# Performance work log

Measured on AMD Instinct MI355X. Metric: run time of the kernel, lower is better.

Reference implementation:

```python
import jax, jax.numpy as jnp
import numpy as np

NUM_HEADS = 16
D_MODEL = 1024
HEAD_DIM = D_MODEL // NUM_HEADS
EPS = 1e-6


def setup_inputs() -> dict:
    key = jax.random.key(0)
    ks = jax.random.split(key, 9)
    B, S, D = 4, 8192, D_MODEL
    scale = 1.0 / np.sqrt(D)  # variance_scaling(1.0, fan_in, normal) approx
    inputs_q = jax.random.normal(ks[0], (B, S, D), dtype=jnp.float32)
    Wq = jax.random.normal(ks[1], (D, D), dtype=jnp.float32) * scale
    Wk = jax.random.normal(ks[2], (D, D), dtype=jnp.float32) * scale
    Wv = jax.random.normal(ks[3], (D, D), dtype=jnp.float32) * scale
    Wo = jax.random.normal(ks[4], (D, D), dtype=jnp.float32) * scale
    bq = jnp.zeros((D,), jnp.float32)
    bk = jnp.zeros((D,), jnp.float32)
    bv = jnp.zeros((D,), jnp.float32)
    bo = jnp.zeros((D,), jnp.float32)
    return {"inputs_q": inputs_q, "Wq": Wq, "bq": bq, "Wk": Wk, "bk": bk,
            "Wv": Wv, "bv": bv, "Wo": Wo, "bo": bo}


def _feature_map(x):
    return jax.nn.elu(x) + 1.0


def reference(inputs_q, Wq, bq, Wk, bk, Wv, bv, Wo, bo):
    B, S, D = inputs_q.shape
    H, Dh = NUM_HEADS, HEAD_DIM
    # QKV projections (self-attention: k,v inputs default to q input)
    q = (inputs_q @ Wq + bq).reshape(B, S, H, Dh)
    k = (inputs_q @ Wk + bk).reshape(B, S, H, Dh)
    v = (inputs_q @ Wv + bv).reshape(B, S, H, Dh)
    q = _feature_map(q)
    k = _feature_map(k)
    # KV outer-product accumulation: [B, H, Dh, Dh]
    kv = jnp.einsum('bkhd,bkhm->bhdm', k, v)
    out = jnp.einsum('bqhd,bhdm->bqhm', q, kv)
    # normalizer: q . sum_k(k)
    normalizer = jnp.einsum('bqhd,bkhd->bqh', q, k)
    normalizer = jnp.maximum(normalizer, EPS)
    out = out / normalizer[..., None]
    out = out.reshape(B, S, D)
    return out @ Wo + bo
```

## Files before the change

kernel.cpp:

```cpp
#include <hip/hip_runtime.h>
#include <cstdint>
#include <cstddef>

#define D_MODEL 1024
#define SEQ 8192

typedef __bf16  bf16x8 __attribute__((ext_vector_type(8)));
typedef short   short8 __attribute__((ext_vector_type(8)));
typedef float   f32x4  __attribute__((ext_vector_type(4)));
typedef unsigned short ushort_t;

__device__ __forceinline__ ushort_t f2bf(float f) {
  uint32_t u = __builtin_bit_cast(uint32_t, f);
  u += 0x7FFFu + ((u >> 16) & 1u);
  return (ushort_t)(u >> 16);
}
__device__ __forceinline__ void gll16(const void* g, void* l) {
  __builtin_amdgcn_global_load_lds(
      (const __attribute__((address_space(1))) void*)g,
      (__attribute__((address_space(3))) void*)l, 16, 0, 0);
}
__device__ __forceinline__ void stage_half(const ushort_t* g, char* l0) {
  gll16(g, l0);
  gll16(g + 65536, l0 + 8192);
}

__global__ void k_convert_x(const float* __restrict__ x, ushort_t* __restrict__ xb, int n) {
  int i = (blockIdx.x * 256 + threadIdx.x) * 8;
  if (i >= n) return;
  float4 v0 = *(const float4*)(x + i);
  float4 v1 = *(const float4*)(x + i + 4);
  ushort_t o[8] = { f2bf(v0.x), f2bf(v0.y), f2bf(v0.z), f2bf(v0.w),
                    f2bf(v1.x), f2bf(v1.y), f2bf(v1.z), f2bf(v1.w) };
  *(short8*)(xb + i) = *(const short8*)o;
}

__global__ void k_transpose_w(const float* W0, const float* W1, const float* W2, const float* W3,
                              ushort_t* Tqkv, ushort_t* To) {
  const float* src; ushort_t* dst;
  switch (blockIdx.z) {
    case 0: src = W0; dst = Tqkv; break;
    case 1: src = W1; dst = Tqkv + (size_t)1024 * 1024; break;
    case 2: src = W2; dst = Tqkv + (size_t)2048 * 1024; break;
    default: src = W3; dst = To; break;
  }
  __shared__ float tile[64][65];
  int tx = threadIdx.x;
  int c = tx & 63, r0 = tx >> 6;
  int bx = blockIdx.x * 64, by = blockIdx.y * 64;
  #pragma unroll
  for (int i = 0; i < 16; i++) {
    int r = i * 4 + r0;
    tile[r][c] = src[(size_t)(by + r) * D_MODEL + bx + c];
  }
  __syncthreads();
  #pragma unroll
  for (int i = 0; i < 16; i++) {
    int r = i * 4 + r0;
    dst[(size_t)(bx + r) * D_MODEL + by + c] = f2bf(tile[c][r]);
  }
}

template<int MODE, int NY>
__global__ __launch_bounds__(512, 2) void k_gemm(const ushort_t* __restrict__ A,
                                                 const ushort_t* __restrict__ Bt,
                                                 const float* __restrict__ b0,
                                                 const float* __restrict__ b1,
                                                 const float* __restrict__ b2,
                                                 ushort_t* __restrict__ o0,
                                                 ushort_t* __restrict__ o1,
                                                 ushort_t* __restrict__ o2,
                                                 float* __restrict__ outf) {
  __shared__ __align__(16) char smem[131072];

  const int nwg = gridDim.x;
  const int bid0 = blockIdx.x;
  const int bid = (bid0 & 7) * (nwg >> 3) + (bid0 >> 3);
  const int xb = bid / NY, yb = bid % NY;
  const int m0 = xb * 256, n0 = yb * 256;

  const int tid = threadIdx.x;
  const int ln = tid & 63;
  const int w  = tid >> 6;
  const int wb = __builtin_amdgcn_readfirstlane(w);
  const int wm = wb >> 2, wn = wb & 3;

  const int srow = wb * 8 + (ln >> 3);
  const int schk = ((ln & 7) ^ ((ln >> 3) & 7)) * 8;
  const ushort_t* gA = A  + (size_t)(m0 + srow) * D_MODEL + schk;
  const ushort_t* gB = Bt + (size_t)(n0 + srow) * D_MODEL + schk;

#define STG_A(BASE, H, T) stage_half(gA + (size_t)(T) * 64 + (size_t)(H) * 131072, smem + (BASE) + (H) * 16384 + wb * 1024)
#define STG_B(BASE, H, T) stage_half(gB + (size_t)(T) * 64 + (size_t)(H) * 131072, smem + (BASE) + 32768 + (H) * 16384 + wb * 1024)

#define VMW_(N) asm volatile("s_waitcnt vmcnt(" #N ")" ::: "memory")
#define VMW(N)  VMW_(N)
#define LGW_(N) asm volatile("s_waitcnt lgkmcnt(" #N ")" ::: "memory")
#define LGW__(N) LGW_(N)
#define LGW(N)  do { LGW__(N); __builtin_amdgcn_sched_barrier(0); } while (0)
#define BARSB { __builtin_amdgcn_s_barrier(); __builtin_amdgcn_sched_barrier(0); }

  f32x4 acc[8][4];
  #pragma unroll
  for (int i = 0; i < 8; i++)
    #pragma unroll
    for (int j = 0; j < 4; j++) acc[i][j] = (f32x4){0.f, 0.f, 0.f, 0.f};
  bf16x8 a0f[4][2], a1f[4][2];
  bf16x8 b0f[2][2], b1f[2][2];

  const int ar  = ln & 15;
  const int cw0 = (((ln >> 4)    ) ^ (ln & 7)) << 4;
  const int cw1 = (((ln >> 4) + 4) ^ (ln & 7)) << 4;

#define LDAH(DST, BASE, MH) { _Pragma("unroll") for (int m_ = 0; m_ < 4; ++m_) { \
    const char* p_ = smem + (BASE) + ((wm * 128 + (MH) * 64 + m_ * 16 + ar) << 7); \
    DST[m_][0] = *(const bf16x8*)(p_ + cw0); DST[m_][1] = *(const bf16x8*)(p_ + cw1); } }
#define LDBH(DST, BASE, NH) { _Pragma("unroll") for (int j_ = 0; j_ < 2; ++j_) { \
    const char* p_ = smem + (BASE) + 32768 + ((wn * 64 + (NH) * 32 + j_ * 16 + ar) << 7); \
    DST[j_][0] = *(const bf16x8*)(p_ + cw0); DST[j_][1] = *(const bf16x8*)(p_ + cw1); } }
#define QUAD(MH, NH, AF, BF) { _Pragma("unroll") for (int m_ = 0; m_ < 4; ++m_) \
    _Pragma("unroll") for (int j_ = 0; j_ < 2; ++j_) { \
      acc[(MH)*4+m_][(NH)*2+j_] = __builtin_amdgcn_mfma_f32_16x16x32_bf16(AF[m_][0], BF[j_][0], acc[(MH)*4+m_][(NH)*2+j_], 0, 0, 0); \
      acc[(MH)*4+m_][(NH)*2+j_] = __builtin_amdgcn_mfma_f32_16x16x32_bf16(AF[m_][1], BF[j_][1], acc[(MH)*4+m_][(NH)*2+j_], 0, 0, 0); } }

#define TILE(T, BT, BN, S1, S2, R1, LP2, LP3) { \
     \
    LDAH(a1f, BT, 1); \
    if (S1) STG_B(BN, 1, (T) + 1); \
    BARSB; \
    LGW(8); \
    __builtin_amdgcn_s_setprio(1); QUAD(0, 0, a0f, b0f); __builtin_amdgcn_s_setprio(0); \
    BARSB; \
     \
    LDBH(b1f, BT, 1); \
    BARSB; \
    LGW(4); \
    __builtin_amdgcn_s_setprio(1); QUAD(1, 0, a1f, b0f); __builtin_amdgcn_s_setprio(0); \
    VMW(0); \
    BARSB; \
     \
    if (R1) LDBH(b0f, BN, 0); \
    if (S2) STG_A(BT, 0, (T) + 2); \
    BARSB; \
    LGW(LP2); \
    __builtin_amdgcn_s_setprio(1); QUAD(0, 1, a0f, b1f); __builtin_amdgcn_s_setprio(0); \
    BARSB; \
     \
    if (R1) LDAH(a0f, BN, 0); \
    if (S2) { STG_A(BT, 1, (T) + 2); STG_B(BT, 0, (T) + 2); } \
    BARSB; \
    LGW(LP3); \
    __builtin_amdgcn_s_setprio(1); QUAD(1, 1, a1f, b1f); __builtin_amdgcn_s_setprio(0); \
    BARSB; \
  }

  STG_A(0, 0, 0); STG_A(0, 1, 0); STG_B(0, 0, 0); STG_B(0, 1, 0);
  STG_A(65536, 0, 1); STG_A(65536, 1, 1); STG_B(65536, 0, 1);
  VMW(6);
  BARSB;
  LDAH(a0f, 0, 0);
  LDBH(b0f, 0, 0);

  #pragma unroll 1
  for (int kt = 0; kt < 14; kt += 2) {
    TILE(kt,     0,     65536, true, true, true, 4, 8);
    TILE(kt + 1, 65536, 0,     true, true, true, 4, 8);
  }
  TILE(14, 0,     65536, true,  false, true,  4, 8);
  TILE(15, 65536, 0,     false, false, false, 0, 0);

#undef STG_A
#undef STG_B
#undef LDAH
#undef LDBH
#undef QUAD
#undef TILE

  const int colb = ln & 15, rowb = (ln >> 4) * 4;

  if constexpr (MODE == 0) {
    const int region = yb >> 2;
    const int nl0 = (yb & 3) * 256;
    const float* bias = region == 0 ? b0 : (region == 1 ? b1 : b2);
    ushort_t* gout    = region == 0 ? o0 : (region == 1 ? o1 : o2);
    const bool act = region < 2;
    ushort_t* Cs = (ushort_t*)smem;
    #pragma unroll
    for (int j = 0; j < 4; ++j) {
      const int col = wn * 64 + j * 16 + colb;
      const float bv_ = bias[nl0 + col];
      #pragma unroll
      for (int i = 0; i < 8; ++i) {
        const int rb_ = wm * 128 + i * 16 + rowb;
        #pragma unroll
        for (int r = 0; r < 4; ++r) {
          float v = acc[i][j][r] + bv_;
          if (act) v = (v > 0.f) ? v + 1.f : __expf(v);
          const int row = rb_ + r;
          const int ch = col >> 3;
          Cs[row * 256 + ((ch ^ (row & 31)) << 3) + (col & 7)] = f2bf(v);
        }
      }
    }
    __syncthreads();
    #pragma unroll
    for (int c = 0; c < 16; ++c) {
      const int idx = c * 512 + tid;
      const int row = idx >> 5, ch = idx & 31;
      short8 t = *(const short8*)&Cs[row * 256 + ((ch ^ (row & 31)) << 3)];
      *(short8*)&gout[(size_t)(m0 + row) * D_MODEL + nl0 + ch * 8] = t;
    }
  } else {
    float* Cf = (float*)smem;
    #pragma unroll
    for (int h = 0; h < 2; ++h) {
      if (h) __syncthreads();
      if (wm == h) {
        #pragma unroll
        for (int j = 0; j < 4; ++j) {
          const int col = wn * 64 + j * 16 + colb;
          const float bv_ = b0[n0 + col];
          #pragma unroll
          for (int i = 0; i < 8; ++i) {
            const int rl = i * 16 + rowb;
            #pragma unroll
            for (int r = 0; r < 4; ++r) {
              const int row = rl + r;
              const int ch = col >> 2;
              Cf[row * 256 + ((ch ^ (row & 7)) << 2) + (col & 3)] = acc[i][j][r] + bv_;
            }
          }
        }
      }
      __syncthreads();
      #pragma unroll
      for (int c = 0; c < 16; ++c) {
        const int idx = c * 512 + tid;
        const int row = idx >> 6, ch = idx & 63;
        float4 t = *(const float4*)&Cf[row * 256 + ((ch ^ (row & 7)) << 2)];
        *(float4*)&outf[(size_t)(m0 + h * 128 + row) * D_MODEL + n0 + ch * 4] = t;
      }
    }
  }
#undef VMW_
#undef VMW
#undef LGW_
#undef LGW__
#undef LGW
#undef BARSB
}

__global__ __launch_bounds__(256) void k_kv_partial(const ushort_t* __restrict__ kmat,
                                                    const ushort_t* __restrict__ vmat,
                                                    float* __restrict__ part) {
  __shared__ __align__(16) ushort_t sbuf[4][2][2][512];
  const int tid = threadIdx.x, ln = tid & 63, w = tid >> 6;
  const int wb = __builtin_amdgcn_readfirstlane(w);
  const int bh = blockIdx.y, chunk = blockIdx.x;
  const int b = bh >> 4, h = bh & 15;
  const size_t cbase = ((size_t)b * SEQ + chunk * 1024 + w * 256) * D_MODEL + h * 64;
  const ushort_t* gk = kmat + cbase + (size_t)(ln >> 3) * D_MODEL + (ln & 7) * 8;
  const ushort_t* gv = vmat + cbase + (size_t)(ln >> 3) * D_MODEL + (ln & 7) * 8;

  float acc[8][8];
  float ksum[8];
  #pragma unroll
  for (int i = 0; i < 8; i++) { ksum[i] = 0.f;
    #pragma unroll
    for (int j = 0; j < 8; j++) acc[i][j] = 0.f; }

  const int r8 = (ln >> 3) * 8, c8 = (ln & 7) * 8;
  gll16(gk, &sbuf[wb][0][0][0]);
  gll16(gv, &sbuf[wb][0][1][0]);
  gk += 8 * D_MODEL; gv += 8 * D_MODEL;

  for (int bt = 0; bt < 32; bt++) {
    const int p = bt & 1;
    if (bt < 31) {
      gll16(gk, &sbuf[wb][p ^ 1][0][0]);
      gll16(gv, &sbuf[wb][p ^ 1][1][0]);
      gk += 8 * D_MODEL; gv += 8 * D_MODEL;
      __builtin_amdgcn_s_waitcnt(0x0F72);
    } else {
      __builtin_amdgcn_s_waitcnt(0x0F70);
    }
    #pragma unroll
    for (int s = 0; s < 8; s++) {
      short8 kk = *(const short8*)&sbuf[wb][p][0][s * 64 + r8];
      short8 vv = *(const short8*)&sbuf[wb][p][1][s * 64 + c8];
      float ka[8], va[8];
      #pragma unroll
      for (int i = 0; i < 8; i++) {
        ka[i] = __builtin_bit_cast(float, (uint32_t)(ushort_t)kk[i] << 16);
        va[i] = __builtin_bit_cast(float, (uint32_t)(ushort_t)vv[i] << 16);
      }
      #pragma unroll
      for (int i = 0; i < 8; i++) {
        ksum[i] += ka[i];
        #pragma unroll
        for (int j = 0; j < 8; j++) acc[i][j] += ka[i] * va[j];
      }
    }
  }
  float* p0 = part + ((size_t)bh * 32 + chunk * 4 + w) * 4160;
  #pragma unroll
  for (int i = 0; i < 8; i++)
    #pragma unroll
    for (int j = 0; j < 8; j++) p0[(r8 + i) * 64 + c8 + j] = acc[i][j];
  if ((ln & 7) == 0) {
    #pragma unroll
    for (int i = 0; i < 8; i++) p0[4096 + r8 + i] = ksum[i];
  }
}

__global__ void k_kv_reduce(const float* __restrict__ part, ushort_t* __restrict__ kvt) {
  const int bh = blockIdx.x, tid = threadIdx.x;
  const float* p0 = part + (size_t)bh * 32 * 4160;
  for (int idx = tid; idx < 4160; idx += 256) {
    float s = 0.f;
    #pragma unroll 4
    for (int c = 0; c < 32; c++) s += p0[(size_t)c * 4160 + idx];
    ushort_t bf = f2bf(s);
    if (idx < 4096) { int d = idx >> 6, m = idx & 63; kvt[(size_t)bh * 4160 + m * 64 + d] = bf; }
    else            { kvt[(size_t)bh * 4160 + 4096 + (idx - 4096)] = bf; }
  }
}

__global__ __launch_bounds__(256) void k_attn(const ushort_t* __restrict__ qmat,
                                              const ushort_t* __restrict__ kvt,
                                              ushort_t* __restrict__ attn) {
  __shared__ __align__(16) ushort_t kvs[65 * 80];
  __shared__ __align__(16) ushort_t qs[4][64 * 80];
  const int tid = threadIdx.x, ln = tid & 63, w = tid >> 6;
  const int bh = blockIdx.y, b = bh >> 4, h = bh & 15;

  for (int idx = tid; idx < 4160; idx += 256) {
    int m = idx >> 6, d = idx & 63;
    kvs[m * 80 + d] = kvt[(size_t)bh * 4160 + idx];
  }
  const size_t s0 = (size_t)b * SEQ + blockIdx.x * 256 + w * 64;
  #pragma unroll
  for (int c = 0; c < 8; c++) {
    int f = c * 64 + ln;
    int row = f >> 3, dg = (f & 7) * 8;
    short8 t = *(const short8*)&qmat[(s0 + row) * D_MODEL + h * 64 + dg];
    *(short8*)&qs[w][row * 80 + dg] = t;
  }
  __syncthreads();

  const int ar = ln & 15, aq = (ln >> 4) * 8;
  f32x4 acc[4][4], nacc[4];
  #pragma unroll
  for (int i = 0; i < 4; i++) { nacc[i] = (f32x4){0.f, 0.f, 0.f, 0.f};
    #pragma unroll
    for (int j = 0; j < 4; j++) acc[i][j] = (f32x4){0.f, 0.f, 0.f, 0.f}; }

  #pragma unroll
  for (int kk = 0; kk < 2; kk++) {
    const int ko = kk * 32 + aq;
    bf16x8 a[4], bb[4], bn;
    #pragma unroll
    for (int i = 0; i < 4; i++) a[i] = *(const bf16x8*)&qs[w][(i * 16 + ar) * 80 + ko];
    #pragma unroll
    for (int j = 0; j < 4; j++) bb[j] = *(const bf16x8*)&kvs[(j * 16 + ar) * 80 + ko];
    bn = *(const bf16x8*)&kvs[64 * 80 + ko];
    #pragma unroll
    for (int i = 0; i < 4; i++) {
      #pragma unroll
      for (int j = 0; j < 4; j++)
        acc[i][j] = __builtin_amdgcn_mfma_f32_16x16x32_bf16(a[i], bb[j], acc[i][j], 0, 0, 0);
      nacc[i] = __builtin_amdgcn_mfma_f32_16x16x32_bf16(a[i], bn, nacc[i], 0, 0, 0);
    }
  }

  const int colb = ln & 15, rowb = (ln >> 4) * 4;
  #pragma unroll
  for (int i = 0; i < 4; i++) {
    #pragma unroll
    for (int r = 0; r < 4; r++) {
      const int row = i * 16 + rowb + r;
      float nm = fmaxf(nacc[i][r], 1e-6f);
      float inv = 1.0f / nm;
      const size_t grow = s0 + row;
      #pragma unroll
      for (int j = 0; j < 4; j++) {
        float v = acc[i][j][r] * inv;
        attn[grow * D_MODEL + h * 64 + j * 16 + colb] = f2bf(v);
      }
    }
  }
}

extern "C" void kernel_launch(void* const* d_in, const int* in_sizes, int n_in,
                              void* d_out, int out_size, void* d_ws, size_t ws_size,
                              hipStream_t stream) {
  const float* x  = (const float*)d_in[0];
  const float* Wq = (const float*)d_in[1];
  const float* bq = (const float*)d_in[2];
  const float* Wk = (const float*)d_in[3];
  const float* bk = (const float*)d_in[4];
  const float* Wv = (const float*)d_in[5];
  const float* bv = (const float*)d_in[6];
  const float* Wo = (const float*)d_in[7];
  const float* bo = (const float*)d_in[8];
  float* out = (float*)d_out;

  const int M = in_sizes[0] / D_MODEL;
  const int B = M / SEQ;
  const int BH = B * 16;

  char* ws = (char*)d_ws;
  size_t off = 0;
  auto alloc = [&](size_t bytes) { char* p = ws + off; off += (bytes + 255) & ~(size_t)255; return p; };
  const size_t mb = (size_t)M * D_MODEL * 2;
  ushort_t* xb    = (ushort_t*)alloc(mb);
  ushort_t* qb    = (ushort_t*)alloc(mb);
  ushort_t* kb    = (ushort_t*)alloc(mb);
  ushort_t* vb    = (ushort_t*)alloc(mb);
  ushort_t* attnb = (ushort_t*)alloc(mb);
  ushort_t* wqkvt = (ushort_t*)alloc((size_t)3 * D_MODEL * D_MODEL * 2);
  ushort_t* wot   = (ushort_t*)alloc((size_t)D_MODEL * D_MODEL * 2);
  ushort_t* kvt   = (ushort_t*)alloc((size_t)BH * 4160 * 2);
  float*    part  = (float*)   alloc((size_t)BH * 32 * 4160 * 4);
  (void)ws_size; (void)n_in; (void)out_size;

  const int n = M * D_MODEL;
  k_convert_x<<<n / (256 * 8), 256, 0, stream>>>(x, xb, n);
  k_transpose_w<<<dim3(16, 16, 4), 256, 0, stream>>>(Wq, Wk, Wv, Wo, wqkvt, wot);

  k_gemm<0, 12><<<(M / 256) * 12, 512, 0, stream>>>(xb, wqkvt, bq, bk, bv, qb, kb, vb, nullptr);

  k_kv_partial<<<dim3(8, BH), 256, 0, stream>>>(kb, vb, part);
  k_kv_reduce<<<BH, 256, 0, stream>>>(part, kvt);
  k_attn<<<dim3(SEQ / 256, BH), 256, 0, stream>>>(qb, kvt, attnb);

  k_gemm<2, 4><<<(M / 256) * 4, 512, 0, stream>>>(attnb, wot, bo, nullptr, nullptr, nullptr, nullptr, nullptr, out);
}
```

Baseline: 807.9 us.

## Restructure GEMM main loop with single A fragment buffer and whole-tile prefetch

Reworks the 256x256 bf16 GEMM k-loop schedule. Each tile now loads its own A and B fragments from LDS at the start instead of prefetching the next tile's fragments during the current one. It keeps a single A fragment register set, reorders the four MFMA quadrants, and issues both halves of the next-next A and B global-to-LDS stages within the tile. This cuts register pressure (fewer fragment buffers) and simplifies wait counts. The cost is that LDS read latency is exposed at the start of each tile, with full lgkmcnt(0) waits before each quadrant.

Measured after the change: 681.6 us. 1.19x faster.

```diff
diff --git a/kernel.cpp b/kernel.cpp
--- a/kernel.cpp
+++ b/kernel.cpp
@@ -95,9 +95,8 @@
 
 #define VMW_(N) asm volatile("s_waitcnt vmcnt(" #N ")" ::: "memory")
 #define VMW(N)  VMW_(N)
-#define LGW_(N) asm volatile("s_waitcnt lgkmcnt(" #N ")" ::: "memory")
-#define LGW__(N) LGW_(N)
-#define LGW(N)  do { LGW__(N); __builtin_amdgcn_sched_barrier(0); } while (0)
+#define LGWC_(N) asm volatile("s_waitcnt lgkmcnt(" #N ")" ::: "memory")
+#define LGW0 do { LGWC_(0); __builtin_amdgcn_sched_barrier(0); } while (0)
 #define BARSB { __builtin_amdgcn_s_barrier(); __builtin_amdgcn_sched_barrier(0); }
 
   f32x4 acc[8][4];
@@ -105,69 +104,67 @@
   for (int i = 0; i < 8; i++)
     #pragma unroll
     for (int j = 0; j < 4; j++) acc[i][j] = (f32x4){0.f, 0.f, 0.f, 0.f};
-  bf16x8 a0f[4][2], a1f[4][2];
-  bf16x8 b0f[2][2], b1f[2][2];
+  bf16x8 af[4][2];
+  bf16x8 bf0[2][2], bf1[2][2];
 
   const int ar  = ln & 15;
   const int cw0 = (((ln >> 4)    ) ^ (ln & 7)) << 4;
   const int cw1 = (((ln >> 4) + 4) ^ (ln & 7)) << 4;
 
-#define LDAH(DST, BASE, MH) { _Pragma("unroll") for (int m_ = 0; m_ < 4; ++m_) { \
+#define LDAH(BASE, MH) { _Pragma("unroll") for (int m_ = 0; m_ < 4; ++m_) { \
     const char* p_ = smem + (BASE) + ((wm * 128 + (MH) * 64 + m_ * 16 + ar) << 7); \
-    DST[m_][0] = *(const bf16x8*)(p_ + cw0); DST[m_][1] = *(const bf16x8*)(p_ + cw1); } }
+    af[m_][0] = *(const bf16x8*)(p_ + cw0); af[m_][1] = *(const bf16x8*)(p_ + cw1); } }
 #define LDBH(DST, BASE, NH) { _Pragma("unroll") for (int j_ = 0; j_ < 2; ++j_) { \
     const char* p_ = smem + (BASE) + 32768 + ((wn * 64 + (NH) * 32 + j_ * 16 + ar) << 7); \
     DST[j_][0] = *(const bf16x8*)(p_ + cw0); DST[j_][1] = *(const bf16x8*)(p_ + cw1); } }
-#define QUAD(MH, NH, AF, BF) { _Pragma("unroll") for (int m_ = 0; m_ < 4; ++m_) \
+#define QUAD(MH, NH, BF) { _Pragma("unroll") for (int m_ = 0; m_ < 4; ++m_) \
     _Pragma("unroll") for (int j_ = 0; j_ < 2; ++j_) { \
-      acc[(MH)*4+m_][(NH)*2+j_] = __builtin_amdgcn_mfma_f32_16x16x32_bf16(AF[m_][0], BF[j_][0], acc[(MH)*4+m_][(NH)*2+j_], 0, 0, 0); \
-      acc[(MH)*4+m_][(NH)*2+j_] = __builtin_amdgcn_mfma_f32_16x16x32_bf16(AF[m_][1], BF[j_][1], acc[(MH)*4+m_][(NH)*2+j_], 0, 0, 0); } }
-
-#define TILE(T, BT, BN, S1, S2, R1, LP2, LP3) { \
+      acc[(MH)*4+m_][(NH)*2+j_] = __builtin_amdgcn_mfma_f32_16x16x32_bf16(af[m_][0], BF[j_][0], acc[(MH)*4+m_][(NH)*2+j_], 0, 0, 0); \
+      acc[(MH)*4+m_][(NH)*2+j_] = __builtin_amdgcn_mfma_f32_16x16x32_bf16(af[m_][1], BF[j_][1], acc[(MH)*4+m_][(NH)*2+j_], 0, 0, 0); } }
+
+#define TILE(T, CUR, S2, VM) { \
      \
-    LDAH(a1f, BT, 1); \
-    if (S1) STG_B(BN, 1, (T) + 1); \
-    BARSB; \
-    LGW(8); \
-    __builtin_amdgcn_s_setprio(1); QUAD(0, 0, a0f, b0f); __builtin_amdgcn_s_setprio(0); \
+    LDAH(CUR, 0); \
+    LDBH(bf0, CUR, 0); \
+    LGWC_(8); \
+    BARSB; \
+    LGW0; \
+    __builtin_amdgcn_s_setprio(1); QUAD(0, 0, bf0); __builtin_amdgcn_s_setprio(0); \
     BARSB; \
      \
-    LDBH(b1f, BT, 1); \
-    BARSB; \
-    LGW(4); \
-    __builtin_amdgcn_s_setprio(1); QUAD(1, 0, a1f, b0f); __builtin_amdgcn_s_setprio(0); \
-    VMW(0); \
+    LDBH(bf1, CUR, 1); \
+    BARSB; \
+    LGW0; \
+    __builtin_amdgcn_s_setprio(1); QUAD(0, 1, bf1); __builtin_amdgcn_s_setprio(0); \
     BARSB; \
      \
-    if (R1) LDBH(b0f, BN, 0); \
-    if (S2) STG_A(BT, 0, (T) + 2); \
-    BARSB; \
-    LGW(LP2); \
-    __builtin_amdgcn_s_setprio(1); QUAD(0, 1, a0f, b1f); __builtin_amdgcn_s_setprio(0); \
+    LDAH(CUR, 1); \
+    if (S2) { STG_B(CUR, 0, (T) + 2); STG_B(CUR, 1, (T) + 2); } \
+    BARSB; \
+    LGW0; \
+    __builtin_amdgcn_s_setprio(1); QUAD(1, 1, bf1); __builtin_amdgcn_s_setprio(0); \
     BARSB; \
      \
-    if (R1) LDAH(a0f, BN, 0); \
-    if (S2) { STG_A(BT, 1, (T) + 2); STG_B(BT, 0, (T) + 2); } \
-    BARSB; \
-    LGW(LP3); \
-    __builtin_amdgcn_s_setprio(1); QUAD(1, 1, a1f, b1f); __builtin_amdgcn_s_setprio(0); \
+    if (S2) { STG_A(CUR, 0, (T) + 2); STG_A(CUR, 1, (T) + 2); } \
+    BARSB; \
+    __builtin_amdgcn_s_setprio(1); QUAD(1, 0, bf0); __builtin_amdgcn_s_setprio(0); \
+    if ((VM) == 0) VMW(8);        \
+    else if ((VM) == 1) VMW(0);   \
     BARSB; \
   }
 
   STG_A(0, 0, 0); STG_A(0, 1, 0); STG_B(0, 0, 0); STG_B(0, 1, 0);
-  STG_A(65536, 0, 1); STG_A(65536, 1, 1); STG_B(65536, 0, 1);
-  VMW(6);
+  STG_A(65536, 0, 1); STG_A(65536, 1, 1); STG_B(65536, 0, 1); STG_B(65536, 1, 1);
+  VMW(8);
   BARSB;
-  LDAH(a0f, 0, 0);
-  LDBH(b0f, 0, 0);
 
   #pragma unroll 1
   for (int kt = 0; kt < 14; kt += 2) {
-    TILE(kt,     0,     65536, true, true, true, 4, 8);
-    TILE(kt + 1, 65536, 0,     true, true, true, 4, 8);
-  }
-  TILE(14, 0,     65536, true,  false, true,  4, 8);
-  TILE(15, 65536, 0,     false, false, false, 0, 0);
+    TILE(kt,     0,     true, 0);
+    TILE(kt + 1, 65536, true, 0);
+  }
+  TILE(14, 0,     false, 1);
+  TILE(15, 65536, false, 2);
 
 #undef STG_A
 #undef STG_B
@@ -244,9 +241,8 @@
   }
 #undef VMW_
 #undef VMW
-#undef LGW_
-#undef LGW__
-#undef LGW
+#undef LGWC_
+#undef LGW0
 #undef BARSB
 }
 
```
